# Kernel tuning notes

Hardware: AMD Instinct MI355X
Metric: run time of the kernel (lower is better)

The kernel has to match this reference:

```python
import jax, jax.numpy as jnp
import numpy as np

B, S, D, H = 4, 2048, 1024, 16
DH = D // H  # head dim = 64

def setup_inputs() -> dict:
    key = jax.random.key(0)
    ks = jax.random.split(key, 11)
    sc = 0.02
    return {
        "Q": jax.random.normal(ks[0], (B, S, D), jnp.float32),
        "K": jax.random.normal(ks[1], (B, S, D), jnp.float32),
        "V": jax.random.normal(ks[2], (B, S, D), jnp.float32),
        "Wq": jax.random.normal(ks[3], (D, D), jnp.float32) * sc,
        "bq": jnp.zeros((D,), jnp.float32),
        "Wk": jax.random.normal(ks[4], (D, D), jnp.float32) * sc,
        "bk": jnp.zeros((D,), jnp.float32),
        "Wv": jax.random.normal(ks[5], (D, D), jnp.float32) * sc,
        "bv": jnp.zeros((D,), jnp.float32),
        "Wo": jax.random.normal(ks[6], (D, D), jnp.float32) * sc,
        "bo": jnp.zeros((D,), jnp.float32),
    }

def reference(Q, K, V, Wq, bq, Wk, bk, Wv, bv, Wo, bo):
    # Linear projections (torch nn.Linear: x @ W.T + b)
    def proj(x, W, b):
        y = x @ W.T + b                      # [B,S,D]
        return y.reshape(B, -1, H, DH).transpose(0, 2, 1, 3)  # [B,H,S,DH]
    q = proj(Q, Wq, bq)
    k = proj(K, Wk, bk)
    v = proj(V, Wv, bv)
    scores = jnp.einsum('bhqd,bhkd->bhqk', q, k) / jnp.sqrt(jnp.float32(DH))
    attn = jax.nn.softmax(scores, axis=-1)   # dropout p=0 -> identity
    ctx = jnp.einsum('bhqk,bhkd->bhqd', attn, v)
    ctx = ctx.transpose(0, 2, 1, 3).reshape(B, -1, D)
    return ctx @ Wo.T + bo
```

## Files before the change

### kernel.cpp

```cpp
#include <hip/hip_runtime.h>
#include <hip/hip_bf16.h>
#include <cmath>

constexpr int kB = 4;
constexpr int kS = 2048;
constexpr int kD = 1024;
constexpr int kH = 16;

typedef __attribute__((ext_vector_type(8))) short bf16x8;
typedef __attribute__((ext_vector_type(4))) float f32x4;
typedef __attribute__((ext_vector_type(4))) unsigned int u32x4;

__device__ __forceinline__ unsigned short f2bf(float f) {
  unsigned int u = __builtin_bit_cast(unsigned int, f);
  u = (u + 0x7fffu + ((u >> 16) & 1u)) >> 16;
  return (unsigned short)u;
}

__device__ __forceinline__ f32x4 mfma16(bf16x8 a, bf16x8 b, f32x4 c) {
  return __builtin_amdgcn_mfma_f32_16x16x32_bf16(a, b, c, 0, 0, 0);
}

#define GL16(gsrc, ldst)                                                      \
  __builtin_amdgcn_global_load_lds(                                           \
      (const __attribute__((address_space(1))) unsigned int*)(gsrc),          \
      (__attribute__((address_space(3))) unsigned int*)(ldst), 16, 0, 0)

#define CVTPK(dst, lo, hi)                                                    \
  asm("v_cvt_pk_bf16_f32 %0, %1, %2" : "=v"(dst) : "v"(lo), "v"(hi))

__global__ __launch_bounds__(256) void cvt_all(
    const float* __restrict__ w0, const float* __restrict__ w1,
    const float* __restrict__ w2, const float* __restrict__ w3,
    const float* __restrict__ x0, const float* __restrict__ x1,
    const float* __restrict__ x2,
    unsigned short* __restrict__ ow0, unsigned short* __restrict__ ow1,
    unsigned short* __restrict__ ow2, unsigned short* __restrict__ ow3,
    unsigned short* __restrict__ ox0, unsigned short* __restrict__ ox1,
    unsigned short* __restrict__ ox2) {
  const int y = blockIdx.y;
  if (y < 4 && blockIdx.x >= 128) return;
  const float* src = y == 0 ? w0 : y == 1 ? w1 : y == 2 ? w2 : y == 3 ? w3
                   : y == 4 ? x0 : y == 5 ? x1 : x2;
  unsigned short* dst = y == 0 ? ow0 : y == 1 ? ow1 : y == 2 ? ow2 : y == 3 ? ow3
                      : y == 4 ? ox0 : y == 5 ? ox1 : ox2;
  __shared__ short Ls[128][72];
  const int pn = blockIdx.x >> 4;
  const int t64 = blockIdx.x & 15;
  const int tid = threadIdx.x;

#pragma unroll
  for (int it = 0; it < 4; ++it) {
    const int u = it * 256 + tid;
    const int row = u >> 3, k8 = u & 7;
    const float* s = src + (size_t)(pn * 128 + row) * kD + t64 * 64 + k8 * 8;
    float4 a = *reinterpret_cast<const float4*>(s);
    float4 b = *reinterpret_cast<const float4*>(s + 4);
    bf16x8 v;
    v[0] = (short)f2bf(a.x); v[1] = (short)f2bf(a.y);
    v[2] = (short)f2bf(a.z); v[3] = (short)f2bf(a.w);
    v[4] = (short)f2bf(b.x); v[5] = (short)f2bf(b.y);
    v[6] = (short)f2bf(b.z); v[7] = (short)f2bf(b.w);
    *reinterpret_cast<bf16x8*>(&Ls[row][k8 * 8]) = v;
  }
  __syncthreads();
#pragma unroll
  for (int it = 0; it < 4; ++it) {
    const int g = it * 256 + tid;
    const int ks8 = g >> 7, row = g & 127;
    bf16x8 v = *reinterpret_cast<const bf16x8*>(&Ls[row][ks8 * 8]);
    const size_t cg = (size_t)pn * 16384 + (size_t)(t64 * 2 + (ks8 >> 2)) * 512 +
                      (ks8 & 3) * 128 + row;
    *reinterpret_cast<bf16x8*>(dst + cg * 8) = v;
  }
}

__global__ __launch_bounds__(512, 4) void proj_gemm4(
    const unsigned short* __restrict__ Xq, const unsigned short* __restrict__ Xk,
    const unsigned short* __restrict__ Xv,
    const unsigned short* __restrict__ Wq, const unsigned short* __restrict__ Wk,
    const unsigned short* __restrict__ Wv,
    const float* __restrict__ bq, const float* __restrict__ bk,
    const float* __restrict__ bv,
    unsigned short* __restrict__ oq, unsigned short* __restrict__ ok,
    unsigned short* __restrict__ ov) {
  const int vmode = blockIdx.z;
  const unsigned short* X = vmode == 0 ? Xq : vmode == 1 ? Xk : Xv;
  const unsigned short* Wb = vmode == 0 ? Wq : vmode == 1 ? Wk : Wv;
  const float* bias = vmode == 0 ? bq : vmode == 1 ? bk : bv;
  unsigned short* out = vmode == 0 ? oq : vmode == 1 ? ok : ov;
  const float scale = vmode == 0 ? 0.18033688f : 1.0f;

  __shared__ short Alds[2][8192];
  __shared__ short Blds[2][4096];
  const int tid = threadIdx.x;
  const int lane = tid & 63;
  const int w = tid >> 6;
  const int wr = w >> 1, wc = w & 1;
  const int lg = lane >> 4, lc = lane & 15;
  const int pm = blockIdx.x;
  const int pn = blockIdx.y;

  auto stage = [&](int bs, int ks) {
#pragma unroll
    for (int it = 0; it < 2; ++it) {
      const int cb = it * 512 + w * 64;
      const int c = cb + lane;
      GL16(X + ((size_t)(2 * pm + (c >> 9)) * 16384 + (size_t)ks * 512 + (c & 511)) * 8,
           &Alds[bs][cb * 8]);
    }
    {
      const int cb = w * 64;
      GL16(Wb + ((size_t)pn * 16384 + (size_t)ks * 512 + cb + lane) * 8,
           &Blds[bs][cb * 8]);
    }
  };

  f32x4 acc[4][4] = {};
  stage(0, 0);
  __syncthreads();
  int cur = 0;

  for (int ks = 0; ks < 32; ++ks) {
    if (ks + 1 < 32) stage(cur ^ 1, ks + 1);
    const short* Ac = &Alds[cur][0];
    const short* Bc = &Blds[cur][0];
    bf16x8 af[4], bfr[4];
#pragma unroll
    for (int mi = 0; mi < 4; ++mi) {
      const int r = wr * 64 + mi * 16 + lc;
      af[mi] = *reinterpret_cast<const bf16x8*>(
          Ac + ((r >> 7) * 512 + lg * 128 + (r & 127)) * 8);
    }
#pragma unroll
    for (int ni = 0; ni < 4; ++ni)
      bfr[ni] = *reinterpret_cast<const bf16x8*>(
          Bc + (lg * 128 + wc * 64 + ni * 16 + lc) * 8);
    __builtin_amdgcn_s_setprio(1);
#pragma unroll
    for (int mi = 0; mi < 4; ++mi)
#pragma unroll
      for (int ni = 0; ni < 4; ++ni)
        acc[mi][ni] = mfma16(af[mi], bfr[ni], acc[mi][ni]);
    __builtin_amdgcn_s_setprio(0);
    __syncthreads();
    cur ^= 1;
  }

#pragma unroll
  for (int mi = 0; mi < 4; ++mi) {
#pragma unroll
    for (int ni = 0; ni < 4; ++ni) {
      const int n = pn * 128 + wc * 64 + ni * 16 + lc;
      const float bv = bias[n];
      const int h = n >> 6, dh = n & 63;
#pragma unroll
      for (int i = 0; i < 4; ++i) {
        const int m = pm * 256 + wr * 64 + mi * 16 + lg * 4 + i;
        const int b = m >> 11, s = m & 2047;
        const float v = (acc[mi][ni][i] + bv) * scale;
        size_t idx;
        if (vmode == 2)
          idx = ((size_t)((b * kH + h) * 256 + (s >> 3))) * 512 + (size_t)dh * 8 + (s & 7);
        else if (vmode == 1)
          idx = ((size_t)((b * kH + h) * kS + s)) * 64 +
                (((dh >> 3) ^ ((s & 3) | (((s >> 3) & 1) << 2))) << 3) + (dh & 7);
        else
          idx = ((size_t)((b * kH + h) * kS + s)) * 64 + dh;
        out[idx] = f2bf(v);
      }
    }
  }
}

__global__ __launch_bounds__(256, 4) void attn_fwd(
    const unsigned short* __restrict__ qh,
    const unsigned short* __restrict__ khs,
    const unsigned short* __restrict__ vs,
    unsigned short* __restrict__ ctx) {
  __shared__ short Kb[2][4096];
  __shared__ short Vb[2][4096];

  const int tid = threadIdx.x;
  const int lane = tid & 63;
  const int w = tid >> 6;
  const int lg = lane >> 4, lc = lane & 15;
  const int bid = blockIdx.x;
  const int wg = (bid & 7) * 128 + (bid >> 3);
  const int qt = wg & 15;
  const int bh = wg >> 4;
  const int q0w = qt * 128 + w * 32;
  const size_t base = (size_t)bh * kS * 64;
  const int krl = 8 * (lc >> 2) + (lc & 3);
  const int kc = (lg ^ ((lc & 3) | (((lc >> 2) & 1) << 2))) << 3;

  const bf16x8 qa00 = *reinterpret_cast<const bf16x8*>(qh + base + (size_t)(q0w + lc) * 64 + lg * 8);
  const bf16x8 qa01 = *reinterpret_cast<const bf16x8*>(qh + base + (size_t)(q0w + lc) * 64 + 32 + lg * 8);
  const bf16x8 qa10 = *reinterpret_cast<const bf16x8*>(qh + base + (size_t)(q0w + 16 + lc) * 64 + lg * 8);
  const bf16x8 qa11 = *reinterpret_cast<const bf16x8*>(qh + base + (size_t)(q0w + 16 + lc) * 64 + 32 + lg * 8);

  f32x4 o0[4] = {}, o1[4] = {};
  float l0 = 0.f, l1 = 0.f;

  auto stage = [&](int bset, int kv0) {
#pragma unroll
    for (int it = 0; it < 2; ++it) {
      const int cb = it * 256 + w * 64;
      GL16(khs + base + (size_t)kv0 * 64 + (size_t)(cb + lane) * 8, &Kb[bset][cb * 8]);
      GL16(vs + base + (size_t)kv0 * 64 + (size_t)(cb + lane) * 8, &Vb[bset][cb * 8]);
    }
  };

  stage(0, 0);
  __syncthreads();
  int cur = 0;

  const f32x4 cinit = {-4.f, -4.f, -4.f, -4.f};

  for (int t = 0; t < 32; ++t) {
    if (t + 1 < 32) stage(cur ^ 1, (t + 1) * 64);
    const short* Kc = &Kb[cur][0];
    const short* Vc = &Vb[cur][0];

#pragma unroll
    for (int kv32 = 0; kv32 < 64; kv32 += 32) {
      f32x4 s00, s01, s10, s11;
      __builtin_amdgcn_s_setprio(1);
      {
        const short* kr = Kc + (kv32 + krl) * 64;
        bf16x8 ka = *reinterpret_cast<const bf16x8*>(kr + kc);
        bf16x8 kb = *reinterpret_cast<const bf16x8*>(kr + (kc ^ 32));
        f32x4 z0 = cinit, z1 = cinit;
        z0 = mfma16(ka, qa00, z0); z0 = mfma16(kb, qa01, z0);
        z1 = mfma16(ka, qa10, z1); z1 = mfma16(kb, qa11, z1);
        s00 = z0; s10 = z1;
      }
      {
        const short* kr = Kc + (kv32 + krl + 4) * 64;
        bf16x8 ka = *reinterpret_cast<const bf16x8*>(kr + kc);
        bf16x8 kb = *reinterpret_cast<const bf16x8*>(kr + (kc ^ 32));
        f32x4 z0 = cinit, z1 = cinit;
        z0 = mfma16(ka, qa00, z0); z0 = mfma16(kb, qa01, z0);
        z1 = mfma16(ka, qa10, z1); z1 = mfma16(kb, qa11, z1);
        s01 = z0; s11 = z1;
      }
      __builtin_amdgcn_s_setprio(0);

      bf16x8 pa0, pa1;
      {
        float pA = __builtin_amdgcn_exp2f(s00[0]);
        float pB = __builtin_amdgcn_exp2f(s00[1]);
        float pC = __builtin_amdgcn_exp2f(s00[2]);
        float pD = __builtin_amdgcn_exp2f(s00[3]);
        float pE = __builtin_amdgcn_exp2f(s01[0]);
        float pF = __builtin_amdgcn_exp2f(s01[1]);
        float pG = __builtin_amdgcn_exp2f(s01[2]);
        float pH = __builtin_amdgcn_exp2f(s01[3]);
        l0 += ((pA + pB) + (pC + pD)) + ((pE + pF) + (pG + pH));
        unsigned uA, uB, uC, uD;
        CVTPK(uA, pA, pB); CVTPK(uB, pC, pD);
        CVTPK(uC, pE, pF); CVTPK(uD, pG, pH);
        u32x4 uu = {uA, uB, uC, uD};
        pa0 = __builtin_bit_cast(bf16x8, uu);
      }
      {
        float pA = __builtin_amdgcn_exp2f(s10[0]);
        float pB = __builtin_amdgcn_exp2f(s10[1]);
        float pC = __builtin_amdgcn_exp2f(s10[2]);
        float pD = __builtin_amdgcn_exp2f(s10[3]);
        float pE = __builtin_amdgcn_exp2f(s11[0]);
        float pF = __builtin_amdgcn_exp2f(s11[1]);
        float pG = __builtin_amdgcn_exp2f(s11[2]);
        float pH = __builtin_amdgcn_exp2f(s11[3]);
        l1 += ((pA + pB) + (pC + pD)) + ((pE + pF) + (pG + pH));
        unsigned uA, uB, uC, uD;
        CVTPK(uA, pA, pB); CVTPK(uB, pC, pD);
        CVTPK(uC, pE, pF); CVTPK(uD, pG, pH);
        u32x4 uu = {uA, uB, uC, uD};
        pa1 = __builtin_bit_cast(bf16x8, uu);
      }

      __builtin_amdgcn_s_setprio(1);
#pragma unroll
      for (int f = 0; f < 4; ++f) {
        bf16x8 vb = *reinterpret_cast<const bf16x8*>(
            Vc + ((kv32 >> 3) + lg) * 512 + (f * 16 + lc) * 8);
        o0[f] = mfma16(pa0, vb, o0[f]);
        o1[f] = mfma16(pa1, vb, o1[f]);
      }
      __builtin_amdgcn_s_setprio(0);
    }
    __syncthreads();
    cur ^= 1;
  }

  l0 += __shfl_xor(l0, 16); l0 += __shfl_xor(l0, 32);
  l1 += __shfl_xor(l1, 16); l1 += __shfl_xor(l1, 32);

  const int b = bh >> 4, h = bh & 15;
#pragma unroll
  for (int i = 0; i < 4; ++i) {
    const float inv0 = 1.0f / __shfl(l0, lg * 4 + i);
    const float inv1 = 1.0f / __shfl(l1, lg * 4 + i);
    const int m0g = b * kS + q0w + lg * 4 + i;
    const int m1g = m0g + 16;
#pragma unroll
    for (int f = 0; f < 4; ++f) {
      const int d = h * 64 + f * 16 + lc;
      const size_t coff = (size_t)(d >> 5) * 512 + ((d >> 3) & 3) * 128;
      ctx[((size_t)(m0g >> 7) * 16384 + coff + (m0g & 127)) * 8 + (d & 7)] =
          f2bf(o0[f][i] * inv0);
      ctx[((size_t)(m1g >> 7) * 16384 + coff + (m1g & 127)) * 8 + (d & 7)] =
          f2bf(o1[f][i] * inv1);
    }
  }
}

__global__ __launch_bounds__(512, 4) void oproj_gemm4(
    const unsigned short* __restrict__ A, const unsigned short* __restrict__ Wb,
    const float* __restrict__ bias, float* __restrict__ out) {
  __shared__ short Alds[2][8192];
  __shared__ short Blds[2][4096];
  const int tid = threadIdx.x;
  const int lane = tid & 63;
  const int w = tid >> 6;
  const int wr = w >> 1, wc = w & 1;
  const int lg = lane >> 4, lc = lane & 15;
  const int pm = blockIdx.x;
  const int pn = blockIdx.y;

  auto stage = [&](int bs, int ks) {
#pragma unroll
    for (int it = 0; it < 2; ++it) {
      const int cb = it * 512 + w * 64;
      const int c = cb + lane;
      GL16(A + ((size_t)(2 * pm + (c >> 9)) * 16384 + (size_t)ks * 512 + (c & 511)) * 8,
           &Alds[bs][cb * 8]);
    }
    {
      const int cb = w * 64;
      GL16(Wb + ((size_t)pn * 16384 + (size_t)ks * 512 + cb + lane) * 8,
           &Blds[bs][cb * 8]);
    }
  };

  f32x4 acc[4][4] = {};
  stage(0, 0);
  __syncthreads();
  int cur = 0;

  for (int ks = 0; ks < 32; ++ks) {
    if (ks + 1 < 32) stage(cur ^ 1, ks + 1);
    const short* Ac = &Alds[cur][0];
    const short* Bc = &Blds[cur][0];
    bf16x8 af[4], bfr[4];
#pragma unroll
    for (int mi = 0; mi < 4; ++mi) {
      const int r = wr * 64 + mi * 16 + lc;
      af[mi] = *reinterpret_cast<const bf16x8*>(
          Ac + ((r >> 7) * 512 + lg * 128 + (r & 127)) * 8);
    }
#pragma unroll
    for (int ni = 0; ni < 4; ++ni)
      bfr[ni] = *reinterpret_cast<const bf16x8*>(
          Bc + (lg * 128 + wc * 64 + ni * 16 + lc) * 8);
    __builtin_amdgcn_s_setprio(1);
#pragma unroll
    for (int mi = 0; mi < 4; ++mi)
#pragma unroll
      for (int ni = 0; ni < 4; ++ni)
        acc[mi][ni] = mfma16(af[mi], bfr[ni], acc[mi][ni]);
    __builtin_amdgcn_s_setprio(0);
    __syncthreads();
    cur ^= 1;
  }

#pragma unroll
  for (int mi = 0; mi < 4; ++mi) {
#pragma unroll
    for (int ni = 0; ni < 4; ++ni) {
      const int n = pn * 128 + wc * 64 + ni * 16 + lc;
      const float bv = bias[n];
#pragma unroll
      for (int i = 0; i < 4; ++i) {
        const long m = (long)pm * 256 + wr * 64 + mi * 16 + lg * 4 + i;
        out[(size_t)m * kD + n] = acc[mi][ni][i] + bv;
      }
    }
  }
}

extern "C" void kernel_launch(void* const* d_in, const int* in_sizes, int n_in,
                              void* d_out, int out_size, void* d_ws, size_t ws_size,
                              hipStream_t stream) {
  const float* Q  = (const float*)d_in[0];
  const float* K  = (const float*)d_in[1];
  const float* V  = (const float*)d_in[2];
  const float* Wq = (const float*)d_in[3];
  const float* bq = (const float*)d_in[4];
  const float* Wk = (const float*)d_in[5];
  const float* bk = (const float*)d_in[6];
  const float* Wv = (const float*)d_in[7];
  const float* bv = (const float*)d_in[8];
  const float* Wo = (const float*)d_in[9];
  const float* bo = (const float*)d_in[10];
  float* out = (float*)d_out;

  const size_t n_tok = (size_t)kB * kS * kD;
  const size_t n_w = (size_t)kD * kD;
  unsigned short* qh  = (unsigned short*)d_ws;
  unsigned short* kh  = qh + n_tok;
  unsigned short* vsw = kh + n_tok;
  unsigned short* xq  = vsw + n_tok;
  unsigned short* xk  = xq + n_tok;
  unsigned short* xv  = xk + n_tok;
  unsigned short* wqb = xv + n_tok;
  unsigned short* wkb = wqb + n_w;
  unsigned short* wvb = wkb + n_w;
  unsigned short* wob = wvb + n_w;
  unsigned short* cx  = xq;

  dim3 b256(256, 1, 1), b512(512, 1, 1);
  cvt_all<<<dim3(1024, 7, 1), b256, 0, stream>>>(Wq, Wk, Wv, Wo, Q, K, V,
                                                 wqb, wkb, wvb, wob, xq, xk, xv);
  proj_gemm4<<<dim3(32, 8, 3), b512, 0, stream>>>(xq, xk, xv, wqb, wkb, wvb,
                                                  bq, bk, bv, qh, kh, vsw);
  attn_fwd<<<dim3(1024, 1, 1), b256, 0, stream>>>(qh, kh, vsw, cx);
  oproj_gemm4<<<dim3(32, 8, 1), b512, 0, stream>>>(cx, wob, bo, out);
}
```

Measured before the change: 200.3 us.

## Triple-buffer LDS in projection GEMMs with partial vmcnt waits

Both projection GEMM kernels move from double to triple buffering of the A/B LDS tiles, prefetching two k-steps ahead. The full __syncthreads drain is replaced by s_waitcnt vmcnt(3) plus a raw barrier, so the next stage's global-to-LDS loads can stay in flight across the barrier. LDS use grows from 48KB to 72KB per block. That may cut occupancy below the launch-bounds target of 4 blocks per CU, and it depends on the vmcnt bookkeeping being correct.

```diff
diff --git a/kernel.cpp b/kernel.cpp
--- a/kernel.cpp
+++ b/kernel.cpp
@@ -28,6 +28,8 @@
 
 #define CVTPK(dst, lo, hi)                                                    \
   asm("v_cvt_pk_bf16_f32 %0, %1, %2" : "=v"(dst) : "v"(lo), "v"(hi))
+
+#define WAITV(n) asm volatile("s_waitcnt vmcnt(" #n ")" ::: "memory")
 
 __global__ __launch_bounds__(256) void cvt_all(
     const float* __restrict__ w0, const float* __restrict__ w1,
@@ -91,8 +93,8 @@
   unsigned short* out = vmode == 0 ? oq : vmode == 1 ? ok : ov;
   const float scale = vmode == 0 ? 0.18033688f : 1.0f;
 
-  __shared__ short Alds[2][8192];
-  __shared__ short Blds[2][4096];
+  __shared__ short Alds[3][8192];
+  __shared__ short Blds[3][4096];
   const int tid = threadIdx.x;
   const int lane = tid & 63;
   const int w = tid >> 6;
@@ -118,11 +120,16 @@
 
   f32x4 acc[4][4] = {};
   stage(0, 0);
-  __syncthreads();
+  stage(1, 1);
+  WAITV(3);
+  __builtin_amdgcn_s_barrier();
   int cur = 0;
 
   for (int ks = 0; ks < 32; ++ks) {
-    if (ks + 1 < 32) stage(cur ^ 1, ks + 1);
+    if (ks + 2 < 32) {
+      int b2 = cur + 2; if (b2 >= 3) b2 -= 3;
+      stage(b2, ks + 2);
+    }
     const short* Ac = &Alds[cur][0];
     const short* Bc = &Blds[cur][0];
     bf16x8 af[4], bfr[4];
@@ -143,8 +150,12 @@
       for (int ni = 0; ni < 4; ++ni)
         acc[mi][ni] = mfma16(af[mi], bfr[ni], acc[mi][ni]);
     __builtin_amdgcn_s_setprio(0);
-    __syncthreads();
-    cur ^= 1;
+
+    if (ks < 31) {
+      if (ks + 2 < 32) WAITV(3); else WAITV(0);
+      __builtin_amdgcn_s_barrier();
+    }
+    cur = cur + 1 == 3 ? 0 : cur + 1;
   }
 
 #pragma unroll
@@ -319,8 +330,8 @@
 __global__ __launch_bounds__(512, 4) void oproj_gemm4(
     const unsigned short* __restrict__ A, const unsigned short* __restrict__ Wb,
     const float* __restrict__ bias, float* __restrict__ out) {
-  __shared__ short Alds[2][8192];
-  __shared__ short Blds[2][4096];
+  __shared__ short Alds[3][8192];
+  __shared__ short Blds[3][4096];
   const int tid = threadIdx.x;
   const int lane = tid & 63;
   const int w = tid >> 6;
@@ -346,11 +357,16 @@
 
   f32x4 acc[4][4] = {};
   stage(0, 0);
-  __syncthreads();
+  stage(1, 1);
+  WAITV(3);
+  __builtin_amdgcn_s_barrier();
   int cur = 0;
 
   for (int ks = 0; ks < 32; ++ks) {
-    if (ks + 1 < 32) stage(cur ^ 1, ks + 1);
+    if (ks + 2 < 32) {
+      int b2 = cur + 2; if (b2 >= 3) b2 -= 3;
+      stage(b2, ks + 2);
+    }
     const short* Ac = &Alds[cur][0];
     const short* Bc = &Blds[cur][0];
     bf16x8 af[4], bfr[4];
@@ -371,8 +387,12 @@
       for (int ni = 0; ni < 4; ++ni)
         acc[mi][ni] = mfma16(af[mi], bfr[ni], acc[mi][ni]);
     __builtin_amdgcn_s_setprio(0);
-    __syncthreads();
-    cur ^= 1;
+
+    if (ks < 31) {
+      if (ks + 2 < 32) WAITV(3); else WAITV(0);
+      __builtin_amdgcn_s_barrier();
+    }
+    cur = cur + 1 == 3 ? 0 : cur + 1;
   }
 
 #pragma unroll
```

New measurement: 201.8 us. Within noise of the previous version (+0.8%).

## Triple-buffer projection GEMM with interleaved loads and finer-grained barriers

Applied to the files above, without the earlier changes.

Rewrites the QKV projection GEMM to use a three-stage LDS ring buffer, so the global-to-LDS loads run two iterations ahead. Each K-step is doubled and split into four phases, each with LDS reads, a slice of prefetch and MFMAs. Raw s_barrier calls with explicit vmcnt/lgkmcnt waits replace __syncthreads. The wave layout changes to 2x4 with 8x2 accumulator tiles, and the launch-bounds occupancy hint drops from 4 to 2 because LDS use roughly triples. The aim is to hide global-load latency and overlap memory traffic with MFMA work, at the cost of lower occupancy and more barriers.

```diff
diff --git a/kernel.cpp b/kernel.cpp
--- a/kernel.cpp
+++ b/kernel.cpp
@@ -28,6 +28,9 @@
 
 #define CVTPK(dst, lo, hi)                                                    \
   asm("v_cvt_pk_bf16_f32 %0, %1, %2" : "=v"(dst) : "v"(lo), "v"(hi))
+
+#define WAITV(n) asm volatile("s_waitcnt vmcnt(" #n ")" ::: "memory")
+#define LGKM0 asm volatile("s_waitcnt lgkmcnt(0)" ::: "memory")
 
 __global__ __launch_bounds__(256) void cvt_all(
     const float* __restrict__ w0, const float* __restrict__ w1,
@@ -75,7 +78,7 @@
   }
 }
 
-__global__ __launch_bounds__(512, 4) void proj_gemm4(
+__global__ __launch_bounds__(512, 2) void proj_gemm5(
     const unsigned short* __restrict__ Xq, const unsigned short* __restrict__ Xk,
     const unsigned short* __restrict__ Xv,
     const unsigned short* __restrict__ Wq, const unsigned short* __restrict__ Wk,
@@ -91,72 +94,125 @@
   unsigned short* out = vmode == 0 ? oq : vmode == 1 ? ok : ov;
   const float scale = vmode == 0 ? 0.18033688f : 1.0f;
 
-  __shared__ short Alds[2][8192];
-  __shared__ short Blds[2][4096];
+  __shared__ short Alds[3][16384];
+  __shared__ short Blds[3][8192];
   const int tid = threadIdx.x;
   const int lane = tid & 63;
   const int w = tid >> 6;
-  const int wr = w >> 1, wc = w & 1;
+  const int wr = w >> 2;
+  const int wn = w & 3;
   const int lg = lane >> 4, lc = lane & 15;
   const int pm = blockIdx.x;
   const int pn = blockIdx.y;
 
-  auto stage = [&](int bs, int ks) {
-#pragma unroll
-    for (int it = 0; it < 2; ++it) {
-      const int cb = it * 512 + w * 64;
-      const int c = cb + lane;
-      GL16(X + ((size_t)(2 * pm + (c >> 9)) * 16384 + (size_t)ks * 512 + (c & 511)) * 8,
-           &Alds[bs][cb * 8]);
-    }
-    {
-      const int cb = w * 64;
-      GL16(Wb + ((size_t)pn * 16384 + (size_t)ks * 512 + cb + lane) * 8,
-           &Blds[bs][cb * 8]);
-    }
-  };
-
-  f32x4 acc[4][4] = {};
-  stage(0, 0);
-  __syncthreads();
+  auto stageA = [&](int bs, int t, int it) {
+    GL16(X + ((size_t)(2 * pm + (it >> 1)) * 16384 +
+              (size_t)(2 * t + (it & 1)) * 512 + w * 64 + lane) * 8,
+         &Alds[bs][(it * 512 + w * 64) * 8]);
+  };
+  auto stageB = [&](int bs, int t, int it) {
+    GL16(Wb + ((size_t)pn * 16384 + (size_t)(2 * t + it) * 512 + w * 64 + lane) * 8,
+         &Blds[bs][(it * 512 + w * 64) * 8]);
+  };
+  auto rdA = [&](const short* Ac, int kk, int mi) {
+    return *reinterpret_cast<const bf16x8*>(
+        Ac + (wr * 1024 + kk * 512 + lg * 128 + mi * 16 + lc) * 8);
+  };
+  auto rdB = [&](const short* Bc, int kk, int ni) {
+    return *reinterpret_cast<const bf16x8*>(
+        Bc + (kk * 512 + lg * 128 + wn * 32 + ni * 16 + lc) * 8);
+  };
+
+  f32x4 acc[8][2] = {};
+
+#pragma unroll
+  for (int it = 0; it < 4; ++it) stageA(0, 0, it);
+#pragma unroll
+  for (int it = 0; it < 2; ++it) stageB(0, 0, it);
+#pragma unroll
+  for (int it = 0; it < 4; ++it) stageA(1, 1, it);
+#pragma unroll
+  for (int it = 0; it < 2; ++it) stageB(1, 1, it);
+  WAITV(6);
+  __builtin_amdgcn_s_barrier();
+
   int cur = 0;
-
-  for (int ks = 0; ks < 32; ++ks) {
-    if (ks + 1 < 32) stage(cur ^ 1, ks + 1);
+  for (int t = 0; t < 16; ++t) {
+    int b2 = cur + 2; if (b2 >= 3) b2 -= 3;
     const short* Ac = &Alds[cur][0];
     const short* Bc = &Blds[cur][0];
-    bf16x8 af[4], bfr[4];
-#pragma unroll
-    for (int mi = 0; mi < 4; ++mi) {
-      const int r = wr * 64 + mi * 16 + lc;
-      af[mi] = *reinterpret_cast<const bf16x8*>(
-          Ac + ((r >> 7) * 512 + lg * 128 + (r & 127)) * 8);
-    }
-#pragma unroll
-    for (int ni = 0; ni < 4; ++ni)
-      bfr[ni] = *reinterpret_cast<const bf16x8*>(
-          Bc + (lg * 128 + wc * 64 + ni * 16 + lc) * 8);
+    const bool pf = (t + 2 < 16);
+    bf16x8 bf0, bf1, a0, a1, a2, a3;
+
+    bf0 = rdB(Bc, 0, 0); bf1 = rdB(Bc, 0, 1);
+    a0 = rdA(Ac, 0, 0); a1 = rdA(Ac, 0, 1);
+    a2 = rdA(Ac, 0, 2); a3 = rdA(Ac, 0, 3);
+    if (pf) { stageA(b2, t + 2, 0); stageA(b2, t + 2, 1); }
+    __builtin_amdgcn_s_barrier();
+    LGKM0;
     __builtin_amdgcn_s_setprio(1);
-#pragma unroll
-    for (int mi = 0; mi < 4; ++mi)
-#pragma unroll
-      for (int ni = 0; ni < 4; ++ni)
-        acc[mi][ni] = mfma16(af[mi], bfr[ni], acc[mi][ni]);
+    acc[0][0] = mfma16(a0, bf0, acc[0][0]); acc[0][1] = mfma16(a0, bf1, acc[0][1]);
+    acc[1][0] = mfma16(a1, bf0, acc[1][0]); acc[1][1] = mfma16(a1, bf1, acc[1][1]);
+    acc[2][0] = mfma16(a2, bf0, acc[2][0]); acc[2][1] = mfma16(a2, bf1, acc[2][1]);
+    acc[3][0] = mfma16(a3, bf0, acc[3][0]); acc[3][1] = mfma16(a3, bf1, acc[3][1]);
     __builtin_amdgcn_s_setprio(0);
-    __syncthreads();
-    cur ^= 1;
-  }
-
-#pragma unroll
-  for (int mi = 0; mi < 4; ++mi) {
-#pragma unroll
-    for (int ni = 0; ni < 4; ++ni) {
-      const int n = pn * 128 + wc * 64 + ni * 16 + lc;
+    __builtin_amdgcn_s_barrier();
+
+    a0 = rdA(Ac, 0, 4); a1 = rdA(Ac, 0, 5);
+    a2 = rdA(Ac, 0, 6); a3 = rdA(Ac, 0, 7);
+    if (pf) { stageA(b2, t + 2, 2); stageA(b2, t + 2, 3); }
+    __builtin_amdgcn_s_barrier();
+    LGKM0;
+    __builtin_amdgcn_s_setprio(1);
+    acc[4][0] = mfma16(a0, bf0, acc[4][0]); acc[4][1] = mfma16(a0, bf1, acc[4][1]);
+    acc[5][0] = mfma16(a1, bf0, acc[5][0]); acc[5][1] = mfma16(a1, bf1, acc[5][1]);
+    acc[6][0] = mfma16(a2, bf0, acc[6][0]); acc[6][1] = mfma16(a2, bf1, acc[6][1]);
+    acc[7][0] = mfma16(a3, bf0, acc[7][0]); acc[7][1] = mfma16(a3, bf1, acc[7][1]);
+    __builtin_amdgcn_s_setprio(0);
+    __builtin_amdgcn_s_barrier();
+
+    bf0 = rdB(Bc, 1, 0); bf1 = rdB(Bc, 1, 1);
+    a0 = rdA(Ac, 1, 0); a1 = rdA(Ac, 1, 1);
+    a2 = rdA(Ac, 1, 2); a3 = rdA(Ac, 1, 3);
+    if (pf) { stageB(b2, t + 2, 0); stageB(b2, t + 2, 1); }
+    __builtin_amdgcn_s_barrier();
+    LGKM0;
+    __builtin_amdgcn_s_setprio(1);
+    acc[0][0] = mfma16(a0, bf0, acc[0][0]); acc[0][1] = mfma16(a0, bf1, acc[0][1]);
+    acc[1][0] = mfma16(a1, bf0, acc[1][0]); acc[1][1] = mfma16(a1, bf1, acc[1][1]);
+    acc[2][0] = mfma16(a2, bf0, acc[2][0]); acc[2][1] = mfma16(a2, bf1, acc[2][1]);
+    acc[3][0] = mfma16(a3, bf0, acc[3][0]); acc[3][1] = mfma16(a3, bf1, acc[3][1]);
+    __builtin_amdgcn_s_setprio(0);
+    __builtin_amdgcn_s_barrier();
+
+    a0 = rdA(Ac, 1, 4); a1 = rdA(Ac, 1, 5);
+    a2 = rdA(Ac, 1, 6); a3 = rdA(Ac, 1, 7);
+    __builtin_amdgcn_s_barrier();
+    LGKM0;
+    __builtin_amdgcn_s_setprio(1);
+    acc[4][0] = mfma16(a0, bf0, acc[4][0]); acc[4][1] = mfma16(a0, bf1, acc[4][1]);
+    acc[5][0] = mfma16(a1, bf0, acc[5][0]); acc[5][1] = mfma16(a1, bf1, acc[5][1]);
+    acc[6][0] = mfma16(a2, bf0, acc[6][0]); acc[6][1] = mfma16(a2, bf1, acc[6][1]);
+    acc[7][0] = mfma16(a3, bf0, acc[7][0]); acc[7][1] = mfma16(a3, bf1, acc[7][1]);
+    __builtin_amdgcn_s_setprio(0);
+
+    if (t < 15) {
+      if (pf) WAITV(6); else WAITV(0);
+      __builtin_amdgcn_s_barrier();
+    }
+    cur = cur + 1 == 3 ? 0 : cur + 1;
+  }
+
+#pragma unroll
+  for (int mi = 0; mi < 8; ++mi) {
+#pragma unroll
+    for (int ni = 0; ni < 2; ++ni) {
+      const int n = pn * 128 + wn * 32 + ni * 16 + lc;
       const float bv = bias[n];
       const int h = n >> 6, dh = n & 63;
 #pragma unroll
       for (int i = 0; i < 4; ++i) {
-        const int m = pm * 256 + wr * 64 + mi * 16 + lg * 4 + i;
+        const int m = pm * 256 + wr * 128 + mi * 16 + lg * 4 + i;
         const int b = m >> 11, s = m & 2047;
         const float v = (acc[mi][ni][i] + bv) * scale;
         size_t idx;
@@ -358,12 +414,13 @@
     for (int mi = 0; mi < 4; ++mi) {
       const int r = wr * 64 + mi * 16 + lc;
       af[mi] = *reinterpret_cast<const bf16x8*>(
-          Ac + ((r >> 7) * 512 + lg * 128 + (r & 127)) * 8);
+          Alds[cur] + ((r >> 7) * 512 + lg * 128 + (r & 127)) * 8);
     }
 #pragma unroll
     for (int ni = 0; ni < 4; ++ni)
       bfr[ni] = *reinterpret_cast<const bf16x8*>(
           Bc + (lg * 128 + wc * 64 + ni * 16 + lc) * 8);
+    (void)Ac;
     __builtin_amdgcn_s_setprio(1);
 #pragma unroll
     for (int mi = 0; mi < 4; ++mi)
@@ -423,7 +480,7 @@
   dim3 b256(256, 1, 1), b512(512, 1, 1);
   cvt_all<<<dim3(1024, 7, 1), b256, 0, stream>>>(Wq, Wk, Wv, Wo, Q, K, V,
                                                  wqb, wkb, wvb, wob, xq, xk, xv);
-  proj_gemm4<<<dim3(32, 8, 3), b512, 0, stream>>>(xq, xk, xv, wqb, wkb, wvb,
+  proj_gemm5<<<dim3(32, 8, 3), b512, 0, stream>>>(xq, xk, xv, wqb, wkb, wvb,
                                                   bq, bk, bv, qh, kh, vsw);
   attn_fwd<<<dim3(1024, 1, 1), b256, 0, stream>>>(qh, kh, vsw, cx);
   oproj_gemm4<<<dim3(32, 8, 1), b512, 0, stream>>>(cx, wob, bo, out);
```

Result: slower. 220.2 us (+9.9%).
